# Kernel tuning notes

Hardware: AMD Instinct MI355X
Metric: run time of the kernel (lower is better)

Reference implementation:

```python
import math
import jax, jax.numpy as jnp
import numpy as np

N = 100000   # nodes
DIN = 128    # in_dim == out_dim
DOUT = 128
H = 8        # heads
HID = 32     # per-head hidden
M = 64       # random features
E = 1600000  # edges
TAU = 0.25
NUM_ITERS = 2
EPS = 1e-6


def _make_projection(m, d, rng):
    # mirrors create_projection_matrix: stacked QR blocks * row-norm multipliers
    blocks = []
    for _ in range(m // d):
        q, _ = np.linalg.qr(rng.standard_normal((d, d)))
        blocks.append(q.T)
    rem = m - (m // d) * d
    if rem > 0:
        q, _ = np.linalg.qr(rng.standard_normal((d, d)))
        blocks.append(q.T[:rem])
    final = np.vstack(blocks)
    mult = np.linalg.norm(rng.standard_normal((m, d)), axis=1)
    return (mult[:, None] * final).astype(np.float32)


def setup_inputs() -> dict:
    key = jax.random.key(0)
    ks = jax.random.split(key, 12)
    x = jax.random.normal(ks[0], (N, DIN), jnp.float32)
    adj = jax.random.randint(ks[1], (2, E), 0, N)
    s1 = 1.0 / math.sqrt(DIN)
    s2 = 1.0 / math.sqrt(H * HID)
    Wq_w = jax.random.uniform(ks[2], (DIN, H * HID), jnp.float32, -s1, s1)
    Wq_b = jax.random.uniform(ks[3], (H * HID,), jnp.float32, -s1, s1)
    Wk_w = jax.random.uniform(ks[4], (DIN, H * HID), jnp.float32, -s1, s1)
    Wk_b = jax.random.uniform(ks[5], (H * HID,), jnp.float32, -s1, s1)
    Wv_w = jax.random.uniform(ks[6], (DIN, H * HID), jnp.float32, -s1, s1)
    Wv_b = jax.random.uniform(ks[7], (H * HID,), jnp.float32, -s1, s1)
    Wo_w = jax.random.uniform(ks[8], (H * HID, DOUT), jnp.float32, -s2, s2)
    Wo_b = jax.random.uniform(ks[9], (DOUT,), jnp.float32, -s2, s2)
    alpha = jnp.zeros((1,), jnp.float32)
    beta = jnp.zeros((1,), jnp.float32)
    proj = jnp.asarray(_make_projection(M, HID, np.random.default_rng(0)))
    return dict(x=x, adj=adj, Wq_w=Wq_w, Wq_b=Wq_b, Wk_w=Wk_w, Wk_b=Wk_b,
                Wv_w=Wv_w, Wv_b=Wv_b, Wo_w=Wo_w, Wo_b=Wo_b,
                alpha=alpha, beta=beta, proj=proj)


def _softmax_kernel(data, is_query, proj):
    # data: [B,N,H,D] -> phi(data): [B,N,H,M]
    d = data.shape[-1]
    data = data * (float(d) ** -0.25)
    ratio = float(proj.shape[0]) ** -0.5
    data_dash = jnp.einsum('bnhd,md->bnhm', data, proj)
    diag = jnp.sum(data * data, axis=-1, keepdims=True) * 0.5
    if is_query:
        mx = jnp.max(data_dash, axis=-1, keepdims=True)
    else:
        mx = jnp.max(jnp.max(data_dash, axis=-1, keepdims=True), axis=1, keepdims=True)
    return ratio * (jnp.exp(data_dash - diag - mx) + EPS)


def reference(x, adj, Wq_w, Wq_b, Wk_w, Wk_b, Wv_w, Wv_b, Wo_w, Wo_b, alpha, beta, proj):
    n = x.shape[0]
    inv_sqrt_tau = 1.0 / math.sqrt(TAU)
    q = (x @ Wq_w + Wq_b).reshape(1, n, H, HID) * inv_sqrt_tau
    k = (x @ Wk_w + Wk_b).reshape(1, n, H, HID) * inv_sqrt_tau
    v = (x @ Wv_w + Wv_b).reshape(1, n, H, HID)
    qp = _softmax_kernel(q, True, proj)    # [1,N,H,M]
    kp = _softmax_kernel(k, False, proj)   # [1,N,H,M]
    # FAVOR+ linear attention: O(N*H*M*D)
    kvs = jnp.einsum('bnhm,bnhd->bhmd', kp, v)
    z_num = jnp.einsum('bnhm,bhmd->bnhd', qp, kvs)
    ks_sum = jnp.sum(kp, axis=1)                      # [1,H,M]
    z_den = jnp.einsum('bnhm,bhm->bnh', qp, ks_sum)   # [1,N,H]
    z_out = z_num / z_den[..., None]                  # [1,N,H,HID]
    x_next = z_out.reshape(n, H * HID) @ Wo_w + Wo_b  # [N,DOUT]
    a = jnp.exp(alpha)
    b = jnp.exp(beta)
    out = x
    for _ in range(NUM_ITERS):
        out = a * out + b * x_next
    return out
```

## Files before the change

### kernel.cpp

```cpp
#include <hip/hip_runtime.h>
#include <math.h>

#define NN 100000
#define SCALE 0.8408964152537145f
#define HALF_SCALE2 0.3535533905932738f
#define RATIO 0.125f
#define KEPS 1e-6f

#define WS_KMAX 0
#define WS_KVSKS 8
#define WS_KVST 16904
#define WS_W2Q 25096
#define WS_W2K 90632
#define WS_B2Q 156168
#define WS_B2K 156680
#define WS_W2QT 157192
#define WS_W2KT 189960
#define WS_WQST 222728
#define WS_WOT 239112
#define WS_BQS 255496
#define WS_WKVT 255752
#define WS_BKV 288520
#define WS_RED2 289032
#define WS_PART 424200

typedef __attribute__((ext_vector_type(8))) short short8;
typedef __attribute__((ext_vector_type(4))) float f32x4;

#define MFMA16(a, b, c) __builtin_amdgcn_mfma_f32_16x16x32_bf16((a), (b), (c), 0, 0, 0)

__device__ __forceinline__ short f2bf(float f) {
    union { float f; unsigned u; } a; a.f = f;
    unsigned r = a.u + 0x7fffu + ((a.u >> 16) & 1u);
    return (short)(r >> 16);
}
__device__ __forceinline__ float bf2f(short s) {
    union { float f; unsigned u; } a; a.u = ((unsigned)(unsigned short)s) << 16;
    return a.f;
}

__device__ __forceinline__ float bsum16(float v) {
    v += __shfl_xor(v, 1); v += __shfl_xor(v, 2);
    v += __shfl_xor(v, 4); v += __shfl_xor(v, 8);
    return v;
}
__device__ __forceinline__ float bmax16(float v) {
    v = fmaxf(v, __shfl_xor(v, 1)); v = fmaxf(v, __shfl_xor(v, 2));
    v = fmaxf(v, __shfl_xor(v, 4)); v = fmaxf(v, __shfl_xor(v, 8));
    return v;
}

__device__ __forceinline__ void atomicMaxFloat(float* addr, float val) {
    int* ai = (int*)addr;
    int cur = *((volatile int*)ai);
    while (val > __int_as_float(cur)) {
        int assumed = cur;
        cur = atomicCAS(ai, assumed, __float_as_int(val));
        if (cur == assumed) break;
    }
}

__global__ __launch_bounds__(256) void fold_kernel(
    const float* __restrict__ Wq_w, const float* __restrict__ Wq_b,
    const float* __restrict__ Wk_w, const float* __restrict__ Wk_b,
    const float* __restrict__ proj, float* __restrict__ ws)
{
    if (blockIdx.x == 0 && threadIdx.x < 8) ws[WS_KMAX + threadIdx.x] = -1e30f;
    int idx = blockIdx.x * 256 + threadIdx.x;
    const int total = 129 * 512;
    if (idx >= 2 * total) return;
    const int mat = (idx >= total) ? 1 : 0;
    idx -= mat * total;
    const int row = idx >> 9;
    const int col = idx & 511;
    const int h = col >> 6, m = col & 63;
    const float* W = mat ? Wk_w : Wq_w;
    const float* b = mat ? Wk_b : Wq_b;
    const float* src = (row < 128) ? (W + row * 256 + h * 32) : (b + h * 32);
    float s = 0.f;
#pragma unroll
    for (int d = 0; d < 32; ++d) s = fmaf(src[d], proj[m * 32 + d], s);
    s *= SCALE;
    if (row < 128) ((short*)(ws + (mat ? WS_W2KT : WS_W2QT)))[col * 128 + row] = f2bf(s);
    else           ws[(mat ? WS_B2K : WS_B2Q) + col] = s;
}

__global__ __launch_bounds__(256) void prep_kernel(
    const float* __restrict__ Wq_w, const float* __restrict__ Wq_b,
    const float* __restrict__ Wk_w, const float* __restrict__ Wk_b,
    const float* __restrict__ Wv_w, const float* __restrict__ Wv_b,
    const float* __restrict__ Wo_w, float* __restrict__ ws)
{
    int idx = blockIdx.x * 256 + threadIdx.x;
    if (idx < 32768) {
        int c = idx >> 7, k = idx & 127;
        ((short*)(ws + WS_WQST))[idx] = f2bf(SCALE * Wq_w[k * 256 + c]);
        return;
    }
    idx -= 32768;
    if (idx < 32768) {
        int o = idx >> 8, c = idx & 255;
        ((short*)(ws + WS_WOT))[idx] = f2bf(Wo_w[c * 128 + o]);
        return;
    }
    idx -= 32768;
    if (idx < 256) { ws[WS_BQS + idx] = SCALE * Wq_b[idx]; return; }
    idx -= 256;
    if (idx < 65536) {
        int c = idx >> 7, k = idx & 127;
        ((short*)(ws + WS_WKVT))[idx] =
            f2bf(c < 256 ? Wk_w[k * 256 + c] : Wv_w[k * 256 + (c - 256)]);
        return;
    }
    idx -= 65536;
    if (idx < 512) ws[WS_BKV + idx] = (idx < 256) ? Wk_b[idx] : Wv_b[idx - 256];
}

__global__ __launch_bounds__(512, 4) void kmax_mfma_kernel(
    const float* __restrict__ x, const float* __restrict__ ws, float* __restrict__ kmax)
{
    __shared__ char smem[16384];
    const short* w2kt = (const short*)(ws + WS_W2KT);
    const float* b2k = ws + WS_B2K;
    const int t = threadIdx.x, w = t >> 6, l = t & 63, lg = l >> 4, li = l & 15;
    float b2r[4];
#pragma unroll
    for (int nc = 0; nc < 4; ++nc) b2r[nc] = b2k[w * 64 + nc * 16 + li];
    short8 Bf[16];
#pragma unroll
    for (int kk = 0; kk < 4; ++kk)
#pragma unroll
        for (int nc = 0; nc < 4; ++nc)
            Bf[kk * 4 + nc] = *(const short8*)&w2kt[(w * 64 + nc * 16 + li) * 128 + kk * 32 + lg * 8];
    float mx = -1e30f;

    for (int tile = blockIdx.x; tile < 1563; tile += gridDim.x) {
        const int n0 = tile * 64;
        __syncthreads();
        {
            const int sr = t >> 3, sp = t & 7;
            float f[16];
            if (n0 + sr < NN) {
                const float* gp = x + (size_t)(n0 + sr) * 128 + sp * 16;
#pragma unroll
                for (int i = 0; i < 4; ++i) {
                    f32x4 v = *(const f32x4*)(gp + i * 4);
                    f[i*4] = v[0]; f[i*4+1] = v[1]; f[i*4+2] = v[2]; f[i*4+3] = v[3];
                }
            } else {
#pragma unroll
                for (int i = 0; i < 16; ++i) f[i] = 0.f;
            }
            const int rb = sr * 256, sw = (sr & 7) << 4;
#pragma unroll
            for (int j = 0; j < 2; ++j) {
                short8 s;
#pragma unroll
                for (int e = 0; e < 8; ++e) s[e] = f2bf(f[j * 8 + e]);
                *(short8*)(smem + rb + ((sp * 32 + 16 * j) ^ sw)) = s;
            }
        }
        __syncthreads();
#pragma unroll
        for (int mr = 0; mr < 4; ++mr) {
            f32x4 acc[4];
#pragma unroll
            for (int nc = 0; nc < 4; ++nc) acc[nc] = (f32x4){0.f, 0.f, 0.f, 0.f};
#pragma unroll
            for (int kk = 0; kk < 4; ++kk) {
                const int row = mr * 16 + li;
                const short8 a = *(const short8*)(smem + row * 256 + (((kk * 32 + lg * 8) * 2) ^ ((row & 7) << 4)));
#pragma unroll
                for (int nc = 0; nc < 4; ++nc) acc[nc] = MFMA16(a, Bf[kk * 4 + nc], acc[nc]);
            }
#pragma unroll
            for (int r = 0; r < 4; ++r) {
                if (n0 + mr * 16 + lg * 4 + r < NN) {
#pragma unroll
                    for (int nc = 0; nc < 4; ++nc) mx = fmaxf(mx, acc[nc][r] + b2r[nc]);
                }
            }
        }
    }
    mx = bmax16(mx); mx = fmaxf(mx, __shfl_xor(mx, 16)); mx = fmaxf(mx, __shfl_xor(mx, 32));
    if (l == 0) atomicMaxFloat(&kmax[w], mx);
}

__global__ __launch_bounds__(512, 2) void kvs_mfma_kernel(
    const float* __restrict__ x, const float* __restrict__ ws,
    float* __restrict__ partials, int nb)
{
    __shared__ char smem[57344];
    const short* wkvt = (const short*)(ws + WS_WKVT);
    const short* w2kt = (const short*)(ws + WS_W2KT);
    const float* bkv  = ws + WS_BKV;
    const float* b2k  = ws + WS_B2K;
    const float* kmaxp = ws + WS_KMAX;

    const int t = threadIdx.x, w = t >> 6, l = t & 63, lg = l >> 4, li = l & 15;
    char* kptb = smem + 8192 + w * 4096;
    char* vtb  = smem + 40960 + w * 2048;
    float bkv_r[4], b2_r[4];
#pragma unroll
    for (int nc = 0; nc < 4; ++nc) {
        bkv_r[nc] = (nc < 2) ? bkv[w * 32 + nc * 16 + li] : bkv[256 + w * 32 + (nc - 2) * 16 + li];
        b2_r[nc]  = b2k[w * 64 + nc * 16 + li];
    }
    const float km = kmaxp[w];

    short8 Bkv[16], B2k[16];
#pragma unroll
    for (int hf = 0; hf < 2; ++hf)
#pragma unroll
        for (int kk = 0; kk < 4; ++kk)
#pragma unroll
            for (int nc = 0; nc < 2; ++nc) {
                const int brow = (hf == 0 ? w * 32 : 256 + w * 32) + nc * 16 + li;
                Bkv[hf * 8 + kk * 2 + nc] = *(const short8*)&wkvt[brow * 128 + kk * 32 + lg * 8];
                B2k[hf * 8 + kk * 2 + nc] =
                    *(const short8*)&w2kt[(w * 64 + (hf * 2 + nc) * 16 + li) * 128 + kk * 32 + lg * 8];
            }

    f32x4 ak[4][2];
#pragma unroll
    for (int mr = 0; mr < 4; ++mr)
#pragma unroll
        for (int nc = 0; nc < 2; ++nc) ak[mr][nc] = (f32x4){0.f,0.f,0.f,0.f};
    float ksacc[4];
#pragma unroll
    for (int nc = 0; nc < 4; ++nc) ksacc[nc] = 0.f;

    for (int tile = blockIdx.x; tile < 3125; tile += nb) {
        const int n0 = tile * 32;
        __syncthreads();
        {
            const int sr = t >> 4, sp = t & 15;
            const float* gp = x + (size_t)(n0 + sr) * 128 + sp * 8;
            f32x4 v0 = *(const f32x4*)gp, v1 = *(const f32x4*)(gp + 4);
            short8 s;
#pragma unroll
            for (int e = 0; e < 4; ++e) { s[e] = f2bf(v0[e]); s[4 + e] = f2bf(v1[e]); }
            *(short8*)(smem + sr * 256 + ((sp * 16) ^ ((sr & 7) << 4))) = s;
        }
        __syncthreads();
        float dgk[2][4];
#pragma unroll
        for (int hf = 0; hf < 2; ++hf) {
            f32x4 acc[2][2];
#pragma unroll
            for (int mr = 0; mr < 2; ++mr)
#pragma unroll
                for (int nc = 0; nc < 2; ++nc) acc[mr][nc] = (f32x4){0.f,0.f,0.f,0.f};
#pragma unroll
            for (int kk = 0; kk < 4; ++kk)
#pragma unroll
                for (int mr = 0; mr < 2; ++mr) {
                    const int row = mr * 16 + li;
                    const short8 a = *(const short8*)(smem + row * 256 + (((kk * 32 + lg * 8) * 2) ^ ((row & 7) << 4)));
#pragma unroll
                    for (int nc = 0; nc < 2; ++nc) acc[mr][nc] = MFMA16(a, Bkv[hf * 8 + kk * 2 + nc], acc[mr][nc]);
                }
            if (hf == 0) {
#pragma unroll
                for (int mr = 0; mr < 2; ++mr)
#pragma unroll
                    for (int r = 0; r < 4; ++r) {
                        const float v0 = acc[mr][0][r] + bkv_r[0];
                        const float v1 = acc[mr][1][r] + bkv_r[1];
                        dgk[mr][r] = HALF_SCALE2 * bsum16(v0 * v0 + v1 * v1);
                    }
            } else {
#pragma unroll
                for (int mr = 0; mr < 2; ++mr)
#pragma unroll
                    for (int nc = 0; nc < 2; ++nc) {
                        short4 s4;
                        s4.x = f2bf(acc[mr][nc][0] + bkv_r[2 + nc]);
                        s4.y = f2bf(acc[mr][nc][1] + bkv_r[2 + nc]);
                        s4.z = f2bf(acc[mr][nc][2] + bkv_r[2 + nc]);
                        s4.w = f2bf(acc[mr][nc][3] + bkv_r[2 + nc]);
                        const int vrow = nc * 16 + li;
                        const int b = 32 * mr + 8 * lg;
                        *(short4*)(vtb + vrow * 64 +
                                   ((((b >> 4) ^ ((vrow >> 1) & 3)) << 4) | (b & 15))) = s4;
                    }
            }
        }
#pragma unroll
        for (int hf = 0; hf < 2; ++hf) {
            f32x4 acd[2][2];
#pragma unroll
            for (int mr = 0; mr < 2; ++mr)
#pragma unroll
                for (int nc = 0; nc < 2; ++nc) acd[mr][nc] = (f32x4){0.f,0.f,0.f,0.f};
#pragma unroll
            for (int kk = 0; kk < 4; ++kk)
#pragma unroll
                for (int mr = 0; mr < 2; ++mr) {
                    const int row = mr * 16 + li;
                    const short8 a = *(const short8*)(smem + row * 256 + (((kk * 32 + lg * 8) * 2) ^ ((row & 7) << 4)));
#pragma unroll
                    for (int nc = 0; nc < 2; ++nc) acd[mr][nc] = MFMA16(a, B2k[hf * 8 + kk * 2 + nc], acd[mr][nc]);
                }
#pragma unroll
            for (int mr = 0; mr < 2; ++mr)
#pragma unroll
                for (int nc = 0; nc < 2; ++nc) {
                    short4 s4;
#pragma unroll
                    for (int r = 0; r < 4; ++r) {
                        const float val = acd[mr][nc][r] + b2_r[hf * 2 + nc];
                        const float kp = RATIO * (__expf(val - dgk[mr][r] - km) + KEPS);
                        const short sb = f2bf(kp);
                        ksacc[hf * 2 + nc] += bf2f(sb);
                        if (r == 0) s4.x = sb; else if (r == 1) s4.y = sb;
                        else if (r == 2) s4.z = sb; else s4.w = sb;
                    }
                    const int mrow = (hf * 2 + nc) * 16 + li;
                    const int b = 32 * mr + 8 * lg;
                    *(short4*)(kptb + mrow * 64 +
                               ((((b >> 4) ^ ((mrow >> 1) & 3)) << 4) | (b & 15))) = s4;
                }
        }
        {
            short8 aa[4], bv[2];
#pragma unroll
            for (int mr = 0; mr < 4; ++mr) {
                const int row = mr * 16 + li;
                aa[mr] = *(const short8*)(kptb + row * 64 + ((lg ^ ((row >> 1) & 3)) << 4));
            }
#pragma unroll
            for (int nc = 0; nc < 2; ++nc) {
                const int vrow = nc * 16 + li;
                bv[nc] = *(const short8*)(vtb + vrow * 64 + ((lg ^ ((vrow >> 1) & 3)) << 4));
            }
#pragma unroll
            for (int mr = 0; mr < 4; ++mr)
#pragma unroll
                for (int nc = 0; nc < 2; ++nc)
                    ak[mr][nc] = MFMA16(aa[mr], bv[nc], ak[mr][nc]);
        }
    }
    float* pb = partials + (size_t)blockIdx.x * 16896;
#pragma unroll
    for (int mr = 0; mr < 4; ++mr)
#pragma unroll
        for (int nc = 0; nc < 2; ++nc)
#pragma unroll
            for (int r = 0; r < 4; ++r) {
                const int m = mr * 16 + lg * 4 + r;
                const int d = nc * 16 + li;
                pb[(w * 64 + m) * 32 + d] = ak[mr][nc][r];
            }
#pragma unroll
    for (int nc = 0; nc < 4; ++nc) {
        float s = ksacc[nc];
        s += __shfl_xor(s, 16); s += __shfl_xor(s, 32);
        if (lg == 0) pb[16384 + w * 64 + nc * 16 + li] = s;
    }
}

__global__ __launch_bounds__(256) void reduce1_kernel(
    const float* __restrict__ partials, float* __restrict__ red2, int nb)
{
    const int b = blockIdx.x;
    const int part = b & 7, grp = b >> 3;
    const int idx = grp * 256 + threadIdx.x;
    if (idx >= 16896) return;
    const int per = (nb + 7) >> 3;
    const int lo = part * per;
    const int hi = (lo + per < nb) ? (lo + per) : nb;
    float s = 0.f;
    for (int q = lo; q < hi; ++q) s += partials[(size_t)q * 16896 + idx];
    red2[part * 16896 + idx] = s;
}

__global__ __launch_bounds__(256) void reduce2_kernel(
    const float* __restrict__ red2, float* __restrict__ ws)
{
    const int idx = blockIdx.x * 256 + threadIdx.x;
    if (idx >= 16896) return;
    float s = 0.f;
#pragma unroll
    for (int p = 0; p < 8; ++p) s += red2[p * 16896 + idx];
    ws[WS_KVSKS + idx] = s;
    if (idx < 16384) {
        const int h = idx >> 11, m = (idx >> 5) & 63, d = idx & 31;
        ((short*)(ws + WS_KVST))[(h * 32 + d) * 64 + m] = f2bf(s);
    }
}

__global__ __launch_bounds__(512, 4) void out_mfma_kernel(
    const float* __restrict__ x, const float* __restrict__ ws,
    const float* __restrict__ alpha, const float* __restrict__ beta,
    const float* __restrict__ Wo_b, float* __restrict__ out)
{
    __shared__ char smem[40960];
    const short* wqst = (const short*)(ws + WS_WQST);
    const short* w2qt = (const short*)(ws + WS_W2QT);
    const short* wot  = (const short*)(ws + WS_WOT);
    const short* kvst = (const short*)(ws + WS_KVST);
    const float* bqs  = ws + WS_BQS;
    const float* b2q  = ws + WS_B2Q;
    const float* ksum = ws + WS_KVSKS + 16384;

    const int t = threadIdx.x, w = t >> 6, l = t & 63, lg = l >> 4, li = l & 15;
    const float a_ = __expf(alpha[0]), b_ = __expf(beta[0]);
    const float a2 = a_ * a_, bc = b_ * (a_ + 1.f);
    char* qpb = smem + 24576 + w * 2048;

    float bq_r[2], b2_r[4], ksv[4];
#pragma unroll
    for (int nc = 0; nc < 2; ++nc) bq_r[nc] = bqs[w * 32 + nc * 16 + li];
#pragma unroll
    for (int nc = 0; nc < 4; ++nc) {
        b2_r[nc] = b2q[w * 64 + nc * 16 + li];
        ksv[nc]  = ksum[w * 64 + nc * 16 + li];
    }
    const float bo = Wo_b[w * 16 + li];

    const int n0 = blockIdx.x * 32;
    f32x4 xr[2];
    {
        const int c4 = (t & 31) * 4;
#pragma unroll
        for (int i = 0; i < 2; ++i) {
            const int sr = (t >> 5) + i * 16;
            xr[i] = *(const f32x4*)(x + (size_t)(n0 + sr) * 128 + c4);
            short4 s4;
            s4.x = f2bf(xr[i][0]); s4.y = f2bf(xr[i][1]);
            s4.z = f2bf(xr[i][2]); s4.w = f2bf(xr[i][3]);
            *(short4*)(smem + sr * 256 + ((c4 * 2) ^ ((sr & 7) << 4))) = s4;
        }
    }
    __syncthreads();
    float dg[2][4];
    {
        short8 Bq[8];
#pragma unroll
        for (int kk = 0; kk < 4; ++kk)
#pragma unroll
            for (int nc = 0; nc < 2; ++nc)
                Bq[kk * 2 + nc] = *(const short8*)&wqst[(w * 32 + nc * 16 + li) * 128 + kk * 32 + lg * 8];
#pragma unroll
        for (int mr = 0; mr < 2; ++mr) {
            f32x4 aq[2];
#pragma unroll
            for (int nc = 0; nc < 2; ++nc) aq[nc] = (f32x4){0.f,0.f,0.f,0.f};
#pragma unroll
            for (int kk = 0; kk < 4; ++kk) {
                const int row = mr * 16 + li;
                const short8 a = *(const short8*)(smem + row * 256 + (((kk * 32 + lg * 8) * 2) ^ ((row & 7) << 4)));
#pragma unroll
                for (int nc = 0; nc < 2; ++nc) aq[nc] = MFMA16(a, Bq[kk * 2 + nc], aq[nc]);
            }
#pragma unroll
            for (int r = 0; r < 4; ++r) {
                const float v0 = aq[0][r] + bq_r[0], v1 = aq[1][r] + bq_r[1];
                dg[mr][r] = 0.5f * bsum16(v0 * v0 + v1 * v1);
            }
        }
    }
    short8 Kf[4];
#pragma unroll
    for (int kk = 0; kk < 2; ++kk)
#pragma unroll
        for (int nc = 0; nc < 2; ++nc)
            Kf[kk * 2 + nc] = *(const short8*)&kvst[(w * 32 + nc * 16 + li) * 64 + kk * 32 + lg * 8];
#pragma unroll
    for (int mr = 0; mr < 2; ++mr) {
        f32x4 ad[4];
#pragma unroll
        for (int hf = 0; hf < 2; ++hf) {
            short8 Bf[8];
#pragma unroll
            for (int kk = 0; kk < 4; ++kk)
#pragma unroll
                for (int nc = 0; nc < 2; ++nc)
                    Bf[kk * 2 + nc] = *(const short8*)&w2qt[(w * 64 + (hf * 2 + nc) * 16 + li) * 128 + kk * 32 + lg * 8];
            f32x4 a0 = (f32x4){0.f,0.f,0.f,0.f}, a1 = (f32x4){0.f,0.f,0.f,0.f};
#pragma unroll
            for (int kk = 0; kk < 4; ++kk) {
                const int row = mr * 16 + li;
                const short8 a = *(const short8*)(smem + row * 256 + (((kk * 32 + lg * 8) * 2) ^ ((row & 7) << 4)));
                a0 = MFMA16(a, Bf[kk * 2 + 0], a0);
                a1 = MFMA16(a, Bf[kk * 2 + 1], a1);
            }
            ad[hf * 2 + 0] = a0; ad[hf * 2 + 1] = a1;
        }
        float zd[4];
#pragma unroll
        for (int r = 0; r < 4; ++r) {
            float vv[4];
#pragma unroll
            for (int nc = 0; nc < 4; ++nc) vv[nc] = ad[nc][r] + b2_r[nc];
            float mx = fmaxf(fmaxf(vv[0], vv[1]), fmaxf(vv[2], vv[3]));
            mx = bmax16(mx);
            const int rr = lg * 4 + r;
            float z = 0.f;
#pragma unroll
            for (int nc = 0; nc < 4; ++nc) {
                const float e = RATIO * (__expf(vv[nc] - dg[mr][r] - mx) + KEPS);
                z = fmaf(e, ksv[nc], z);
                const unsigned pe = (unsigned)(unsigned short)f2bf(e);
                const unsigned po = (unsigned)__shfl_xor((int)pe, 1);
                if (!(li & 1))
                    *(unsigned*)(qpb + rr * 128 +
                        ((nc * 32 + 2 * li) ^ ((rr & 7) << 4))) = pe | (po << 16);
            }
            zd[r] = bsum16(z);
        }
        f32x4 az[2];
#pragma unroll
        for (int nc = 0; nc < 2; ++nc) az[nc] = (f32x4){0.f,0.f,0.f,0.f};
#pragma unroll
        for (int kk = 0; kk < 2; ++kk) {
            const short8 aa = *(const short8*)(qpb + li * 128 +
                              ((kk * 64 + lg * 16) ^ ((li & 7) << 4)));
#pragma unroll
            for (int nc = 0; nc < 2; ++nc) az[nc] = MFMA16(aa, Kf[kk * 2 + nc], az[nc]);
        }
#pragma unroll
        for (int nc = 0; nc < 2; ++nc)
#pragma unroll
            for (int r = 0; r < 4; ++r) {
                const int row = mr * 16 + lg * 4 + r;
                const float zv = az[nc][r] / zd[r];
                const unsigned pe = (unsigned)(unsigned short)f2bf(zv);
                const unsigned po = (unsigned)__shfl_xor((int)pe, 1);
                if (!(li & 1))
                    *(unsigned*)(smem + 8192 + row * 512 +
                        ((2 * (w * 32 + nc * 16 + li)) ^ ((row & 7) << 4))) = pe | (po << 16);
            }
    }
    short8 Bo[8];
#pragma unroll
    for (int kk = 0; kk < 8; ++kk)
        Bo[kk] = *(const short8*)&wot[(w * 16 + li) * 256 + kk * 32 + lg * 8];
    __syncthreads();
    f32x4 ao[2];
#pragma unroll
    for (int mr = 0; mr < 2; ++mr) ao[mr] = (f32x4){0.f,0.f,0.f,0.f};
#pragma unroll
    for (int mr = 0; mr < 2; ++mr)
#pragma unroll
        for (int kk = 0; kk < 8; ++kk) {
            const int row = mr * 16 + li;
            const short8 aa = *(const short8*)(smem + 8192 + row * 512 +
                              ((kk * 64 + lg * 16) ^ ((row & 7) << 4)));
            ao[mr] = MFMA16(aa, Bo[kk], ao[mr]);
        }
    __syncthreads();
    float* xnb = (float*)smem;
#pragma unroll
    for (int mr = 0; mr < 2; ++mr)
#pragma unroll
        for (int r = 0; r < 4; ++r) {
            const int row = mr * 16 + lg * 4 + r;
            xnb[row * 132 + w * 16 + li] = ao[mr][r] + bo;
        }
    __syncthreads();
    {
        const int c4 = (t & 31) * 4;
#pragma unroll
        for (int i = 0; i < 2; ++i) {
            const int sr = (t >> 5) + i * 16;
            const f32x4 xn4 = *(const f32x4*)&xnb[sr * 132 + c4];
            f32x4 o4;
            o4[0] = a2 * xr[i][0] + bc * xn4[0];
            o4[1] = a2 * xr[i][1] + bc * xn4[1];
            o4[2] = a2 * xr[i][2] + bc * xn4[2];
            o4[3] = a2 * xr[i][3] + bc * xn4[3];
            *(f32x4*)(out + (size_t)(n0 + sr) * 128 + c4) = o4;
        }
    }
}

extern "C" void kernel_launch(void* const* d_in, const int* in_sizes, int n_in,
                              void* d_out, int out_size, void* d_ws, size_t ws_size,
                              hipStream_t stream) {
    (void)in_sizes; (void)n_in; (void)out_size;
    const float* x    = (const float*)d_in[0];
    const float* Wq_w = (const float*)d_in[2];
    const float* Wq_b = (const float*)d_in[3];
    const float* Wk_w = (const float*)d_in[4];
    const float* Wk_b = (const float*)d_in[5];
    const float* Wv_w = (const float*)d_in[6];
    const float* Wv_b = (const float*)d_in[7];
    const float* Wo_w = (const float*)d_in[8];
    const float* Wo_b = (const float*)d_in[9];
    const float* alpha= (const float*)d_in[10];
    const float* beta = (const float*)d_in[11];
    const float* proj = (const float*)d_in[12];
    float* out = (float*)d_out;
    float* ws  = (float*)d_ws;

    float* kmax     = ws + WS_KMAX;
    float* red2     = ws + WS_RED2;
    float* partials = ws + WS_PART;
    const size_t availf = (ws_size / 4 > (size_t)WS_PART) ? (ws_size / 4 - WS_PART) : 0;
    int nb = (int)(availf / 16896);
    if (nb > 256) nb = 256;
    if (nb < 1) nb = 1;

    fold_kernel<<<516, 256, 0, stream>>>(Wq_w, Wq_b, Wk_w, Wk_b, proj, ws);
    prep_kernel<<<515, 256, 0, stream>>>(Wq_w, Wq_b, Wk_w, Wk_b, Wv_w, Wv_b, Wo_w, ws);
    kmax_mfma_kernel<<<512, 512, 0, stream>>>(x, ws, kmax);
    kvs_mfma_kernel<<<nb, 512, 0, stream>>>(x, ws, partials, nb);
    reduce1_kernel<<<528, 256, 0, stream>>>(partials, red2, nb);
    reduce2_kernel<<<66, 256, 0, stream>>>(red2, ws);
    out_mfma_kernel<<<3125, 512, 0, stream>>>(x, ws, alpha, beta, Wo_b, out);
}
```

Measured before the change: 316.8 us.

## Replace separate key-max pass with online running-max rescaling in KVS kernel

Removes the dedicated kmax kernel, which streamed all of x and ran a full MFMA projection just to find the global per-head key max. The KVS kernel now keeps a running max per block, rescaling its accumulators when the max grows, and emits per-block maxima. A new single-block reduce0 computes per-block rescale factors that reduce1 applies. The EPS term is added analytically from accumulated V sums and the node count. The q-feature and z stores in the output kernel were also changed from shuffle-packed pairs to plain 16-bit LDS stores. The cost is extra exp/rescale work inside the KVS loop and one extra tiny launch.

```diff
diff --git a/kernel.cpp b/kernel.cpp
--- a/kernel.cpp
+++ b/kernel.cpp
@@ -6,12 +6,12 @@
 #define HALF_SCALE2 0.3535533905932738f
 #define RATIO 0.125f
 #define KEPS 1e-6f
+#define PSTR 17160
+#define RSTR 17152
 
 #define WS_KMAX 0
 #define WS_KVSKS 8
 #define WS_KVST 16904
-#define WS_W2Q 25096
-#define WS_W2K 90632
 #define WS_B2Q 156168
 #define WS_B2K 156680
 #define WS_W2QT 157192
@@ -22,7 +22,8 @@
 #define WS_WKVT 255752
 #define WS_BKV 288520
 #define WS_RED2 289032
-#define WS_PART 424200
+#define WS_SCAL 426248
+#define WS_PART 428296
 
 typedef __attribute__((ext_vector_type(8))) short short8;
 typedef __attribute__((ext_vector_type(4))) float f32x4;
@@ -48,16 +49,6 @@
     v = fmaxf(v, __shfl_xor(v, 1)); v = fmaxf(v, __shfl_xor(v, 2));
     v = fmaxf(v, __shfl_xor(v, 4)); v = fmaxf(v, __shfl_xor(v, 8));
     return v;
-}
-
-__device__ __forceinline__ void atomicMaxFloat(float* addr, float val) {
-    int* ai = (int*)addr;
-    int cur = *((volatile int*)ai);
-    while (val > __int_as_float(cur)) {
-        int assumed = cur;
-        cur = atomicCAS(ai, assumed, __float_as_int(val));
-        if (cur == assumed) break;
-    }
 }
 
 __global__ __launch_bounds__(256) void fold_kernel(
@@ -65,7 +56,6 @@
     const float* __restrict__ Wk_w, const float* __restrict__ Wk_b,
     const float* __restrict__ proj, float* __restrict__ ws)
 {
-    if (blockIdx.x == 0 && threadIdx.x < 8) ws[WS_KMAX + threadIdx.x] = -1e30f;
     int idx = blockIdx.x * 256 + threadIdx.x;
     const int total = 129 * 512;
     if (idx >= 2 * total) return;
@@ -116,76 +106,6 @@
     if (idx < 512) ws[WS_BKV + idx] = (idx < 256) ? Wk_b[idx] : Wv_b[idx - 256];
 }
 
-__global__ __launch_bounds__(512, 4) void kmax_mfma_kernel(
-    const float* __restrict__ x, const float* __restrict__ ws, float* __restrict__ kmax)
-{
-    __shared__ char smem[16384];
-    const short* w2kt = (const short*)(ws + WS_W2KT);
-    const float* b2k = ws + WS_B2K;
-    const int t = threadIdx.x, w = t >> 6, l = t & 63, lg = l >> 4, li = l & 15;
-    float b2r[4];
-#pragma unroll
-    for (int nc = 0; nc < 4; ++nc) b2r[nc] = b2k[w * 64 + nc * 16 + li];
-    short8 Bf[16];
-#pragma unroll
-    for (int kk = 0; kk < 4; ++kk)
-#pragma unroll
-        for (int nc = 0; nc < 4; ++nc)
-            Bf[kk * 4 + nc] = *(const short8*)&w2kt[(w * 64 + nc * 16 + li) * 128 + kk * 32 + lg * 8];
-    float mx = -1e30f;
-
-    for (int tile = blockIdx.x; tile < 1563; tile += gridDim.x) {
-        const int n0 = tile * 64;
-        __syncthreads();
-        {
-            const int sr = t >> 3, sp = t & 7;
-            float f[16];
-            if (n0 + sr < NN) {
-                const float* gp = x + (size_t)(n0 + sr) * 128 + sp * 16;
-#pragma unroll
-                for (int i = 0; i < 4; ++i) {
-                    f32x4 v = *(const f32x4*)(gp + i * 4);
-                    f[i*4] = v[0]; f[i*4+1] = v[1]; f[i*4+2] = v[2]; f[i*4+3] = v[3];
-                }
-            } else {
-#pragma unroll
-                for (int i = 0; i < 16; ++i) f[i] = 0.f;
-            }
-            const int rb = sr * 256, sw = (sr & 7) << 4;
-#pragma unroll
-            for (int j = 0; j < 2; ++j) {
-                short8 s;
-#pragma unroll
-                for (int e = 0; e < 8; ++e) s[e] = f2bf(f[j * 8 + e]);
-                *(short8*)(smem + rb + ((sp * 32 + 16 * j) ^ sw)) = s;
-            }
-        }
-        __syncthreads();
-#pragma unroll
-        for (int mr = 0; mr < 4; ++mr) {
-            f32x4 acc[4];
-#pragma unroll
-            for (int nc = 0; nc < 4; ++nc) acc[nc] = (f32x4){0.f, 0.f, 0.f, 0.f};
-#pragma unroll
-            for (int kk = 0; kk < 4; ++kk) {
-                const int row = mr * 16 + li;
-                const short8 a = *(const short8*)(smem + row * 256 + (((kk * 32 + lg * 8) * 2) ^ ((row & 7) << 4)));
-#pragma unroll
-                for (int nc = 0; nc < 4; ++nc) acc[nc] = MFMA16(a, Bf[kk * 4 + nc], acc[nc]);
-            }
-#pragma unroll
-            for (int r = 0; r < 4; ++r) {
-                if (n0 + mr * 16 + lg * 4 + r < NN) {
-#pragma unroll
-                    for (int nc = 0; nc < 4; ++nc) mx = fmaxf(mx, acc[nc][r] + b2r[nc]);
-                }
-            }
-        }
-    }
-    mx = bmax16(mx); mx = fmaxf(mx, __shfl_xor(mx, 16)); mx = fmaxf(mx, __shfl_xor(mx, 32));
-    if (l == 0) atomicMaxFloat(&kmax[w], mx);
-}
-
 __global__ __launch_bounds__(512, 2) void kvs_mfma_kernel(
     const float* __restrict__ x, const float* __restrict__ ws,
     float* __restrict__ partials, int nb)
@@ -195,7 +115,6 @@
     const short* w2kt = (const short*)(ws + WS_W2KT);
     const float* bkv  = ws + WS_BKV;
     const float* b2k  = ws + WS_B2K;
-    const float* kmaxp = ws + WS_KMAX;
 
     const int t = threadIdx.x, w = t >> 6, l = t & 63, lg = l >> 4, li = l & 15;
     char* kptb = smem + 8192 + w * 4096;
@@ -206,7 +125,6 @@
         bkv_r[nc] = (nc < 2) ? bkv[w * 32 + nc * 16 + li] : bkv[256 + w * 32 + (nc - 2) * 16 + li];
         b2_r[nc]  = b2k[w * 64 + nc * 16 + li];
     }
-    const float km = kmaxp[w];
 
     short8 Bkv[16], B2k[16];
 #pragma unroll
@@ -229,6 +147,9 @@
     float ksacc[4];
 #pragma unroll
     for (int nc = 0; nc < 4; ++nc) ksacc[nc] = 0.f;
+    float svacc[2];
+    svacc[0] = 0.f; svacc[1] = 0.f;
+    float m_run = -1e30f;
 
     for (int tile = blockIdx.x; tile < 3125; tile += nb) {
         const int n0 = tile * 32;
@@ -275,10 +196,12 @@
 #pragma unroll
                     for (int nc = 0; nc < 2; ++nc) {
                         short4 s4;
-                        s4.x = f2bf(acc[mr][nc][0] + bkv_r[2 + nc]);
-                        s4.y = f2bf(acc[mr][nc][1] + bkv_r[2 + nc]);
-                        s4.z = f2bf(acc[mr][nc][2] + bkv_r[2 + nc]);
-                        s4.w = f2bf(acc[mr][nc][3] + bkv_r[2 + nc]);
+                        float vv0 = acc[mr][nc][0] + bkv_r[2 + nc];
+                        float vv1 = acc[mr][nc][1] + bkv_r[2 + nc];
+                        float vv2 = acc[mr][nc][2] + bkv_r[2 + nc];
+                        float vv3 = acc[mr][nc][3] + bkv_r[2 + nc];
+                        svacc[nc] += (vv0 + vv1) + (vv2 + vv3);
+                        s4.x = f2bf(vv0); s4.y = f2bf(vv1); s4.z = f2bf(vv2); s4.w = f2bf(vv3);
                         const int vrow = nc * 16 + li;
                         const int b = 32 * mr + 8 * lg;
                         *(short4*)(vtb + vrow * 64 +
@@ -286,6 +209,7 @@
                     }
             }
         }
+        float vals[2][2][2][4];
 #pragma unroll
         for (int hf = 0; hf < 2; ++hf) {
             f32x4 acd[2][2];
@@ -305,13 +229,42 @@
 #pragma unroll
             for (int mr = 0; mr < 2; ++mr)
 #pragma unroll
+                for (int nc = 0; nc < 2; ++nc)
+#pragma unroll
+                    for (int r = 0; r < 4; ++r)
+                        vals[hf][mr][nc][r] = acd[mr][nc][r] + b2_r[hf * 2 + nc];
+        }
+        float tm = -1e30f;
+#pragma unroll
+        for (int hf = 0; hf < 2; ++hf)
+#pragma unroll
+            for (int mr = 0; mr < 2; ++mr)
+#pragma unroll
+                for (int nc = 0; nc < 2; ++nc)
+#pragma unroll
+                    for (int r = 0; r < 4; ++r) tm = fmaxf(tm, vals[hf][mr][nc][r]);
+        tm = bmax16(tm); tm = fmaxf(tm, __shfl_xor(tm, 16)); tm = fmaxf(tm, __shfl_xor(tm, 32));
+        if (tm > m_run) {
+            const float s = __expf(m_run - tm);
+#pragma unroll
+            for (int mr = 0; mr < 4; ++mr)
+#pragma unroll
+                for (int nc = 0; nc < 2; ++nc) ak[mr][nc] *= s;
+#pragma unroll
+            for (int nc = 0; nc < 4; ++nc) ksacc[nc] *= s;
+            m_run = tm;
+        }
+#pragma unroll
+        for (int hf = 0; hf < 2; ++hf)
+#pragma unroll
+            for (int mr = 0; mr < 2; ++mr)
+#pragma unroll
                 for (int nc = 0; nc < 2; ++nc) {
                     short4 s4;
 #pragma unroll
                     for (int r = 0; r < 4; ++r) {
-                        const float val = acd[mr][nc][r] + b2_r[hf * 2 + nc];
-                        const float kp = RATIO * (__expf(val - dgk[mr][r] - km) + KEPS);
-                        const short sb = f2bf(kp);
+                        const float e = RATIO * __expf(vals[hf][mr][nc][r] - dgk[mr][r] - m_run);
+                        const short sb = f2bf(e);
                         ksacc[hf * 2 + nc] += bf2f(sb);
                         if (r == 0) s4.x = sb; else if (r == 1) s4.y = sb;
                         else if (r == 2) s4.z = sb; else s4.w = sb;
@@ -321,7 +274,6 @@
                     *(short4*)(kptb + mrow * 64 +
                                ((((b >> 4) ^ ((mrow >> 1) & 3)) << 4) | (b & 15))) = s4;
                 }
-        }
         {
             short8 aa[4], bv[2];
 #pragma unroll
@@ -341,7 +293,7 @@
                     ak[mr][nc] = MFMA16(aa[mr], bv[nc], ak[mr][nc]);
         }
     }
-    float* pb = partials + (size_t)blockIdx.x * 16896;
+    float* pb = partials + (size_t)blockIdx.x * PSTR;
 #pragma unroll
     for (int mr = 0; mr < 4; ++mr)
 #pragma unroll
@@ -358,21 +310,53 @@
         s += __shfl_xor(s, 16); s += __shfl_xor(s, 32);
         if (lg == 0) pb[16384 + w * 64 + nc * 16 + li] = s;
     }
+#pragma unroll
+    for (int nc = 0; nc < 2; ++nc) {
+        float sv = svacc[nc];
+        sv += __shfl_xor(sv, 16); sv += __shfl_xor(sv, 32);
+        if (lg == 0) pb[16896 + w * 32 + nc * 16 + li] = sv;
+    }
+    if (l == 0) pb[17152 + w] = m_run;
+}
+
+__global__ __launch_bounds__(256) void reduce0_kernel(
+    const float* __restrict__ partials, float* __restrict__ scal, int nb)
+{
+    __shared__ float kmS[8];
+    const int t = threadIdx.x;
+    if (t < 8) {
+        float m = -1e30f;
+        for (int q = 0; q < nb; ++q) m = fmaxf(m, partials[(size_t)q * PSTR + 17152 + t]);
+        kmS[t] = m;
+    }
+    __syncthreads();
+    for (int i = t; i < nb * 8; i += 256) {
+        const int q = i >> 3, h = i & 7;
+        scal[i] = __expf(partials[(size_t)q * PSTR + 17152 + h] - kmS[h]);
+    }
 }
 
 __global__ __launch_bounds__(256) void reduce1_kernel(
-    const float* __restrict__ partials, float* __restrict__ red2, int nb)
+    const float* __restrict__ partials, const float* __restrict__ scal,
+    float* __restrict__ red2, int nb)
 {
     const int b = blockIdx.x;
     const int part = b & 7, grp = b >> 3;
     const int idx = grp * 256 + threadIdx.x;
-    if (idx >= 16896) return;
+    if (idx >= RSTR) return;
     const int per = (nb + 7) >> 3;
     const int lo = part * per;
     const int hi = (lo + per < nb) ? (lo + per) : nb;
+    int h = 0; bool scaled = true;
+    if (idx < 16384) h = idx >> 11;
+    else if (idx < 16896) h = (idx - 16384) >> 6;
+    else scaled = false;
     float s = 0.f;
-    for (int q = lo; q < hi; ++q) s += partials[(size_t)q * 16896 + idx];
-    red2[part * 16896 + idx] = s;
+    for (int q = lo; q < hi; ++q) {
+        const float p = partials[(size_t)q * PSTR + idx];
+        s += scaled ? p * scal[q * 8 + h] : p;
+    }
+    red2[(size_t)part * RSTR + idx] = s;
 }
 
 __global__ __launch_bounds__(256) void reduce2_kernel(
@@ -382,11 +366,21 @@
     if (idx >= 16896) return;
     float s = 0.f;
 #pragma unroll
-    for (int p = 0; p < 8; ++p) s += red2[p * 16896 + idx];
-    ws[WS_KVSKS + idx] = s;
+    for (int p = 0; p < 8; ++p) s += red2[(size_t)p * RSTR + idx];
+    float val;
+    if (idx < 16384) {
+        const int h = idx >> 11, d = idx & 31;
+        float sv = 0.f;
+#pragma unroll
+        for (int p = 0; p < 8; ++p) sv += red2[(size_t)p * RSTR + 16896 + h * 32 + d];
+        val = s + RATIO * KEPS * sv;
+    } else {
+        val = s + RATIO * KEPS * 100000.0f;
+    }
+    ws[WS_KVSKS + idx] = val;
     if (idx < 16384) {
         const int h = idx >> 11, m = (idx >> 5) & 63, d = idx & 31;
-        ((short*)(ws + WS_KVST))[(h * 32 + d) * 64 + m] = f2bf(s);
+        ((short*)(ws + WS_KVST))[(h * 32 + d) * 64 + m] = f2bf(val);
     }
 }
 
@@ -497,16 +491,13 @@
             float mx = fmaxf(fmaxf(vv[0], vv[1]), fmaxf(vv[2], vv[3]));
             mx = bmax16(mx);
             const int rr = lg * 4 + r;
+            const int sw = (rr & 7) << 4;
             float z = 0.f;
 #pragma unroll
             for (int nc = 0; nc < 4; ++nc) {
                 const float e = RATIO * (__expf(vv[nc] - dg[mr][r] - mx) + KEPS);
                 z = fmaf(e, ksv[nc], z);
-                const unsigned pe = (unsigned)(unsigned short)f2bf(e);
-                const unsigned po = (unsigned)__shfl_xor((int)pe, 1);
-                if (!(li & 1))
-                    *(unsigned*)(qpb + rr * 128 +
-                        ((nc * 32 + 2 * li) ^ ((rr & 7) << 4))) = pe | (po << 16);
+                *(short*)(qpb + rr * 128 + ((nc * 32 + 2 * li) ^ sw)) = f2bf(e);
             }
             zd[r] = bsum16(z);
         }
@@ -526,11 +517,8 @@
             for (int r = 0; r < 4; ++r) {
                 const int row = mr * 16 + lg * 4 + r;
                 const float zv = az[nc][r] / zd[r];
-                const unsigned pe = (unsigned)(unsigned short)f2bf(zv);
-                const unsigned po = (unsigned)__shfl_xor((int)pe, 1);
-                if (!(li & 1))
-                    *(unsigned*)(smem + 8192 + row * 512 +
-                        ((2 * (w * 32 + nc * 16 + li)) ^ ((row & 7) << 4))) = pe | (po << 16);
+                *(short*)(smem + 8192 + row * 512 +
+                    ((2 * (w * 32 + nc * 16 + li)) ^ ((row & 7) << 4))) = f2bf(zv);
             }
     }
     short8 Bo[8];
@@ -595,19 +583,19 @@
     float* out = (float*)d_out;
     float* ws  = (float*)d_ws;
 
-    float* kmax     = ws + WS_KMAX;
     float* red2     = ws + WS_RED2;
+    float* scal     = ws + WS_SCAL;
     float* partials = ws + WS_PART;
     const size_t availf = (ws_size / 4 > (size_t)WS_PART) ? (ws_size / 4 - WS_PART) : 0;
-    int nb = (int)(availf / 16896);
+    int nb = (int)(availf / PSTR);
     if (nb > 256) nb = 256;
     if (nb < 1) nb = 1;
 
     fold_kernel<<<516, 256, 0, stream>>>(Wq_w, Wq_b, Wk_w, Wk_b, proj, ws);
     prep_kernel<<<515, 256, 0, stream>>>(Wq_w, Wq_b, Wk_w, Wk_b, Wv_w, Wv_b, Wo_w, ws);
-    kmax_mfma_kernel<<<512, 512, 0, stream>>>(x, ws, kmax);
     kvs_mfma_kernel<<<nb, 512, 0, stream>>>(x, ws, partials, nb);
-    reduce1_kernel<<<528, 256, 0, stream>>>(partials, red2, nb);
+    reduce0_kernel<<<1, 256, 0, stream>>>(partials, scal, nb);
+    reduce1_kernel<<<536, 256, 0, stream>>>(partials, scal, red2, nb);
     reduce2_kernel<<<66, 256, 0, stream>>>(red2, ws);
     out_mfma_kernel<<<3125, 512, 0, stream>>>(x, ws, alpha, beta, Wo_b, out);
 }
```

After: 333.5 us. 5.3% more time.
